# Optimization experiments

Measured on AMD Instinct MI355X. Metric: run time of the kernel, lower is better.

Reference implementation:

```python
import jax, jax.numpy as jnp
import numpy as np
from jax import lax

T_STEPS = 8

def _dwconv(x, kernel):
    # depthwise conv, NHWC input, HWIO kernel with I=1, groups=C
    C = x.shape[-1]
    return lax.conv_general_dilated(
        x, kernel, window_strides=(1, 1), padding='SAME',
        dimension_numbers=('NHWC', 'HWIO', 'NHWC'), feature_group_count=C)

def setup_inputs() -> dict:
    key = jax.random.key(0)
    k1, k2, k3 = jax.random.split(key, 3)
    B, H, W, C, k = 8, 128, 128, 256, 7
    x = jax.random.normal(k1, (B, H, W, C), dtype=jnp.float32)
    A_kernel = 0.02 * jax.random.normal(k2, (k, k, 1, C), dtype=jnp.float32)
    B_kernel = 0.02 * jax.random.normal(k3, (k, k, 1, C), dtype=jnp.float32)
    return {'x': x, 'A_kernel': A_kernel, 'B_kernel': B_kernel}

def reference(x, A_kernel, B_kernel):
    # SSM recurrence h_t = A * h_{t-1} + B * x  (depthwise spatial convs)
    A_stable = 0.9 * jnp.tanh(A_kernel)
    Bx = _dwconv(x, B_kernel)  # precomputed input drive, (B,H,W,C)

    def step(h, _):
        return _dwconv(h, A_stable) + Bx, None

    h0 = jnp.zeros_like(x)
    h_final, _ = lax.scan(step, h0, None, length=T_STEPS)
    return h_final
```

## Files before the change

kernel.cpp:

```cpp
#include <hip/hip_runtime.h>
#include <cmath>

#define HH    128
#define WW    128
#define CCH   256
#define BATCH 8
#define NPLANE (BATCH*CCH)
#define PLANE_ELEMS (HH*WW)

#define TB   3
#define STR  136
#define S4   34
#define HPAD 134
#define PLANE_LDS (HPAD*STR)

template<int SAVE_BX>
__device__ __forceinline__ void conv_pass(const float* src, float* dst,
                                          const float* cf, float* bx,
                                          int tx, int ty)
{
    const int x4 = tx * 2;
    const int y0 = ty * 8;
    __align__(16) float wd[7][16];
    const float4* s4 = (const float4*)src;
    float4* d4 = (float4*)dst;

#pragma unroll
    for (int r = 0; r < 7; r++) {
        const float4* row = s4 + (y0 + r) * S4 + x4;
        float4 a = row[0], b = row[1], c = row[2], d = row[3];
        *(float4*)&wd[r][0]  = a;  *(float4*)&wd[r][4]  = b;
        *(float4*)&wd[r][8]  = c;  *(float4*)&wd[r][12] = d;
    }

#pragma unroll
    for (int o = 0; o < 8; o++) {
        if (o > 0) {
            const int slot = (o + 6) % 7;
            const float4* row = s4 + (y0 + o + 6) * S4 + x4;
            float4 a = row[0], b = row[1], c = row[2], d = row[3];
            *(float4*)&wd[slot][0]  = a;  *(float4*)&wd[slot][4]  = b;
            *(float4*)&wd[slot][8]  = c;  *(float4*)&wd[slot][12] = d;
        }
        float acc[8];
#pragma unroll
        for (int i = 0; i < 8; i++) acc[i] = SAVE_BX ? 0.0f : bx[o * 8 + i];
#pragma unroll
        for (int ky = 0; ky < 7; ky++) {
            const int s = (o + ky) % 7;
#pragma unroll
            for (int kx = 0; kx < 7; kx++) {
                const float k = cf[ky * 7 + kx];
#pragma unroll
                for (int i = 0; i < 8; i++)
                    acc[i] = fmaf(wd[s][i + kx + 1], k, acc[i]);
            }
        }
        if (SAVE_BX) {
#pragma unroll
            for (int i = 0; i < 8; i++) bx[o * 8 + i] = acc[i];
        }
        float4 lo = make_float4(acc[0], acc[1], acc[2], acc[3]);
        float4 hi = make_float4(acc[4], acc[5], acc[6], acc[7]);
        float4* drow = d4 + (y0 + o + TB) * S4 + (tx * 2 + 1);
        drow[0] = lo;
        drow[1] = hi;
    }
}

__global__ __launch_bounds__(256, 1) void ssm_kernel(float* planes,
                                                     const float* __restrict__ Ak,
                                                     const float* __restrict__ Bk)
{
    __shared__ float buf[2 * PLANE_LDS];
    const int p  = blockIdx.x;
    const int c  = p & (CCH - 1);
    const int t  = threadIdx.x;
    const int tx = t & 15, ty = t >> 4;

    float4* z = (float4*)buf;
    const int n4 = 2 * PLANE_LDS / 4;
    for (int i = t; i < n4; i += 256) z[i] = make_float4(0.f, 0.f, 0.f, 0.f);

    float bco[49];
#pragma unroll
    for (int i = 0; i < 49; i++) bco[i] = Bk[i * CCH + c];

    __syncthreads();

    const float4* gx = (const float4*)planes + (size_t)p * (PLANE_ELEMS / 4);
#pragma unroll
    for (int i = 0; i < 16; i++) {
        int idx = i * 256 + t, y = idx >> 5, xc = idx & 31;
        ((float4*)buf)[(y + TB) * S4 + xc + 1] = gx[idx];
    }
    __syncthreads();

    float bx[64];
    conv_pass<1>(buf, buf + PLANE_LDS, bco, bx, tx, ty);

    float aco[49];
#pragma unroll
    for (int i = 0; i < 49; i++) {
        float v = 0.9f * tanhf(Ak[i * CCH + c]);
        aco[i] = __uint_as_float(__builtin_amdgcn_readfirstlane(__float_as_uint(v)));
    }
    __syncthreads();

    for (int s = 0; s < 7; s++) {
        const float* src = buf + (1 - (s & 1)) * PLANE_LDS;
        float* dst       = buf + (s & 1) * PLANE_LDS;
        conv_pass<0>(src, dst, aco, bx, tx, ty);
        __syncthreads();
    }

    float4* gout = (float4*)planes + (size_t)p * (PLANE_ELEMS / 4);
#pragma unroll
    for (int i = 0; i < 16; i++) {
        int idx = i * 256 + t, y = idx >> 5, xc = idx & 31;
        gout[idx] = ((float4*)buf)[(y + TB) * S4 + xc + 1];
    }
}

__global__ __launch_bounds__(256) void transpose_in(const float* __restrict__ x,
                                                    float* __restrict__ xt)
{
    __shared__ float tile[64][65];
    const int p = blockIdx.x;
    const int b = p >> 10, rem = p & 1023, thw = rem >> 2, tc = rem & 3;
    const int t = threadIdx.x;
    const int m = t & 15, g = t >> 4;

    const size_t inbase = ((size_t)(b * 16384 + thw * 64)) * 256 + tc * 64;
#pragma unroll
    for (int i = 0; i < 4; i++) {
        int r = i * 16 + g;
        float4 v = *(const float4*)(x + inbase + (size_t)r * 256 + m * 4);
        tile[r][m * 4 + 0] = v.x; tile[r][m * 4 + 1] = v.y;
        tile[r][m * 4 + 2] = v.z; tile[r][m * 4 + 3] = v.w;
    }
    __syncthreads();
    const size_t outbase = ((size_t)(b * 256 + tc * 64)) * 16384 + thw * 64;
#pragma unroll
    for (int i = 0; i < 4; i++) {
        int cr = i * 16 + g;
        float4 v = make_float4(tile[m * 4 + 0][cr], tile[m * 4 + 1][cr],
                               tile[m * 4 + 2][cr], tile[m * 4 + 3][cr]);
        *(float4*)(xt + outbase + (size_t)cr * 16384 + m * 4) = v;
    }
}

__global__ __launch_bounds__(256) void transpose_out(const float* __restrict__ ht,
                                                     float* __restrict__ out)
{
    __shared__ float tile[64][65];
    const int p = blockIdx.x;
    const int b = p >> 10, rem = p & 1023, thw = rem >> 2, tc = rem & 3;
    const int t = threadIdx.x;
    const int m = t & 15, g = t >> 4;

    const size_t inbase = ((size_t)(b * 256 + tc * 64)) * 16384 + thw * 64;
#pragma unroll
    for (int i = 0; i < 4; i++) {
        int cr = i * 16 + g;
        float4 v = *(const float4*)(ht + inbase + (size_t)cr * 16384 + m * 4);
        tile[cr][m * 4 + 0] = v.x; tile[cr][m * 4 + 1] = v.y;
        tile[cr][m * 4 + 2] = v.z; tile[cr][m * 4 + 3] = v.w;
    }
    __syncthreads();
    const size_t outbase = ((size_t)(b * 16384 + thw * 64)) * 256 + tc * 64;
#pragma unroll
    for (int i = 0; i < 4; i++) {
        int r = i * 16 + g;
        float4 v = make_float4(tile[m * 4 + 0][r], tile[m * 4 + 1][r],
                               tile[m * 4 + 2][r], tile[m * 4 + 3][r]);
        *(float4*)(out + outbase + (size_t)r * 256 + m * 4) = v;
    }
}

extern "C" void kernel_launch(void* const* d_in, const int* in_sizes, int n_in,
                              void* d_out, int out_size, void* d_ws, size_t ws_size,
                              hipStream_t stream)
{
    (void)in_sizes; (void)n_in; (void)out_size; (void)ws_size;
    const float* x  = (const float*)d_in[0];
    const float* Ak = (const float*)d_in[1];
    const float* Bk = (const float*)d_in[2];
    float* out    = (float*)d_out;
    float* planes = (float*)d_ws;

    transpose_in <<<8192, 256, 0, stream>>>(x, planes);
    ssm_kernel   <<<NPLANE, 256, 0, stream>>>(planes, Ak, Bk);
    transpose_out<<<8192, 256, 0, stream>>>(planes, out);
}
```

Measured before the change: 689.7 us.

## Single-buffer LDS with register staging to fit two blocks per CU

Switches the per-plane recurrence from two LDS buffers to one: each thread computes a 16x4 output tile into registers, syncs, then writes it back into the shared plane. The halved LDS footprint and launch bounds of 2 are meant to allow two blocks per CU so one block's LDS traffic can overlap the other's math. The final step writes straight from registers to global memory. The narrower 4-wide tile reloads more halo per output, and holding 64 bx plus 64 hn values per thread raises register pressure, which could cause spills.

```diff
diff --git a/kernel.cpp b/kernel.cpp
--- a/kernel.cpp
+++ b/kernel.cpp
@@ -14,77 +14,85 @@
 #define HPAD 134
 #define PLANE_LDS (HPAD*STR)
 
-template<int SAVE_BX>
-__device__ __forceinline__ void conv_pass(const float* src, float* dst,
-                                          const float* cf, float* bx,
-                                          int tx, int ty)
-{
-    const int x4 = tx * 2;
-    const int y0 = ty * 8;
-    __align__(16) float wd[7][16];
-    const float4* s4 = (const float4*)src;
-    float4* d4 = (float4*)dst;
+template<int INIT0>
+__device__ __forceinline__ void conv16(const float* sbuf, const float* cf,
+                                       const float* accin, float* out,
+                                       int tx, int ty)
+{
+    const int xq = tx;
+    const int y0 = ty * 16;
+    __align__(16) float wd[7][12];
+    const float4* s4 = (const float4*)sbuf;
 
 #pragma unroll
     for (int r = 0; r < 7; r++) {
-        const float4* row = s4 + (y0 + r) * S4 + x4;
-        float4 a = row[0], b = row[1], c = row[2], d = row[3];
-        *(float4*)&wd[r][0]  = a;  *(float4*)&wd[r][4]  = b;
-        *(float4*)&wd[r][8]  = c;  *(float4*)&wd[r][12] = d;
-    }
-
-#pragma unroll
-    for (int o = 0; o < 8; o++) {
+        const float4* row = s4 + (y0 + r) * S4 + xq;
+        float4 a = row[0], b = row[1], c = row[2];
+        *(float4*)&wd[r][0] = a; *(float4*)&wd[r][4] = b; *(float4*)&wd[r][8] = c;
+    }
+
+#pragma unroll
+    for (int o = 0; o < 16; o++) {
         if (o > 0) {
             const int slot = (o + 6) % 7;
-            const float4* row = s4 + (y0 + o + 6) * S4 + x4;
-            float4 a = row[0], b = row[1], c = row[2], d = row[3];
-            *(float4*)&wd[slot][0]  = a;  *(float4*)&wd[slot][4]  = b;
-            *(float4*)&wd[slot][8]  = c;  *(float4*)&wd[slot][12] = d;
+            const float4* row = s4 + (y0 + o + 6) * S4 + xq;
+            float4 a = row[0], b = row[1], c = row[2];
+            *(float4*)&wd[slot][0] = a; *(float4*)&wd[slot][4] = b;
+            *(float4*)&wd[slot][8] = c;
         }
-        float acc[8];
-#pragma unroll
-        for (int i = 0; i < 8; i++) acc[i] = SAVE_BX ? 0.0f : bx[o * 8 + i];
+        float a0, a1, a2, a3;
+        if (INIT0) { a0 = a1 = a2 = a3 = 0.0f; }
+        else { a0 = accin[o*4+0]; a1 = accin[o*4+1]; a2 = accin[o*4+2]; a3 = accin[o*4+3]; }
 #pragma unroll
         for (int ky = 0; ky < 7; ky++) {
             const int s = (o + ky) % 7;
 #pragma unroll
             for (int kx = 0; kx < 7; kx++) {
                 const float k = cf[ky * 7 + kx];
-#pragma unroll
-                for (int i = 0; i < 8; i++)
-                    acc[i] = fmaf(wd[s][i + kx + 1], k, acc[i]);
+                a0 = fmaf(wd[s][0 + kx + 1], k, a0);
+                a1 = fmaf(wd[s][1 + kx + 1], k, a1);
+                a2 = fmaf(wd[s][2 + kx + 1], k, a2);
+                a3 = fmaf(wd[s][3 + kx + 1], k, a3);
             }
         }
-        if (SAVE_BX) {
-#pragma unroll
-            for (int i = 0; i < 8; i++) bx[o * 8 + i] = acc[i];
-        }
-        float4 lo = make_float4(acc[0], acc[1], acc[2], acc[3]);
-        float4 hi = make_float4(acc[4], acc[5], acc[6], acc[7]);
-        float4* drow = d4 + (y0 + o + TB) * S4 + (tx * 2 + 1);
-        drow[0] = lo;
-        drow[1] = hi;
-    }
-}
-
-__global__ __launch_bounds__(256, 1) void ssm_kernel(float* planes,
+        out[o*4+0] = a0; out[o*4+1] = a1; out[o*4+2] = a2; out[o*4+3] = a3;
+    }
+}
+
+__device__ __forceinline__ void tile_to_lds(float* sbuf, const float* v,
+                                            int tx, int ty)
+{
+    float4* d4 = (float4*)sbuf;
+    const int y0 = ty * 16;
+#pragma unroll
+    for (int o = 0; o < 16; o++) {
+        d4[(y0 + o + TB) * S4 + tx + 1] =
+            make_float4(v[o*4+0], v[o*4+1], v[o*4+2], v[o*4+3]);
+    }
+}
+
+__global__ __launch_bounds__(256, 2) void ssm_kernel(float* planes,
                                                      const float* __restrict__ Ak,
                                                      const float* __restrict__ Bk)
 {
-    __shared__ float buf[2 * PLANE_LDS];
+    __shared__ float buf[PLANE_LDS];
     const int p  = blockIdx.x;
     const int c  = p & (CCH - 1);
     const int t  = threadIdx.x;
-    const int tx = t & 15, ty = t >> 4;
-
-    float4* z = (float4*)buf;
-    const int n4 = 2 * PLANE_LDS / 4;
-    for (int i = t; i < n4; i += 256) z[i] = make_float4(0.f, 0.f, 0.f, 0.f);
+    const int tx = t & 31, ty = t >> 5;
+
+    {
+        float4* z = (float4*)buf;
+        for (int i = t; i < PLANE_LDS / 4; i += 256)
+            z[i] = make_float4(0.f, 0.f, 0.f, 0.f);
+    }
 
     float bco[49];
 #pragma unroll
-    for (int i = 0; i < 49; i++) bco[i] = Bk[i * CCH + c];
+    for (int i = 0; i < 49; i++) {
+        float v = Bk[i * CCH + c];
+        bco[i] = __uint_as_float(__builtin_amdgcn_readfirstlane(__float_as_uint(v)));
+    }
 
     __syncthreads();
 
@@ -97,7 +105,7 @@
     __syncthreads();
 
     float bx[64];
-    conv_pass<1>(buf, buf + PLANE_LDS, bco, bx, tx, ty);
+    conv16<1>(buf, bco, nullptr, bx, tx, ty);
 
     float aco[49];
 #pragma unroll
@@ -105,20 +113,28 @@
         float v = 0.9f * tanhf(Ak[i * CCH + c]);
         aco[i] = __uint_as_float(__builtin_amdgcn_readfirstlane(__float_as_uint(v)));
     }
-    __syncthreads();
-
-    for (int s = 0; s < 7; s++) {
-        const float* src = buf + (1 - (s & 1)) * PLANE_LDS;
-        float* dst       = buf + (s & 1) * PLANE_LDS;
-        conv_pass<0>(src, dst, aco, bx, tx, ty);
+
+    __syncthreads();
+    tile_to_lds(buf, bx, tx, ty);
+    __syncthreads();
+
+    float hn[64];
+    for (int s = 0; s < 6; s++) {
+        conv16<0>(buf, aco, bx, hn, tx, ty);
         __syncthreads();
-    }
-
-    float4* gout = (float4*)planes + (size_t)p * (PLANE_ELEMS / 4);
-#pragma unroll
-    for (int i = 0; i < 16; i++) {
-        int idx = i * 256 + t, y = idx >> 5, xc = idx & 31;
-        gout[idx] = ((float4*)buf)[(y + TB) * S4 + xc + 1];
+        tile_to_lds(buf, hn, tx, ty);
+        __syncthreads();
+    }
+
+    conv16<0>(buf, aco, bx, hn, tx, ty);
+    {
+        float4* gout = (float4*)planes + (size_t)p * (PLANE_ELEMS / 4);
+        const int y0 = ty * 16;
+#pragma unroll
+        for (int o = 0; o < 16; o++) {
+            gout[(y0 + o) * 32 + tx] =
+                make_float4(hn[o*4+0], hn[o*4+1], hn[o*4+2], hn[o*4+3]);
+        }
     }
 }
 
```

After: 1.059 ms. +53.5%, slower.

## Use 512 threads per plane with 4-wide outputs and fuse final conv into store

Applied to the files above, without the earlier changes.

Doubles the threads per block to 512, so each thread computes 4 output columns instead of 8. This shrinks the sliding register window and the per-thread bx storage to lift occupancy and parallelism. The last recurrence step now writes straight to global memory instead of going through LDS and a separate copy-out loop. The cost is more redundant LDS window loads per output, since each 4-wide tile reloads 12 floats per row, and a higher thread count contending for the same LDS.

```diff
diff --git a/kernel.cpp b/kernel.cpp
--- a/kernel.cpp
+++ b/kernel.cpp
@@ -14,61 +14,54 @@
 #define HPAD 134
 #define PLANE_LDS (HPAD*STR)
 
-template<int SAVE_BX>
-__device__ __forceinline__ void conv_pass(const float* src, float* dst,
-                                          const float* cf, float* bx,
-                                          int tx, int ty)
+template<int MODE>
+__device__ __forceinline__ void conv8(const float* src, float* dstl, float4* gout,
+                                      const float* cf, float* bx, int tx, int ty)
 {
-    const int x4 = tx * 2;
     const int y0 = ty * 8;
-    __align__(16) float wd[7][16];
+    __align__(16) float wd[7][12];
     const float4* s4 = (const float4*)src;
-    float4* d4 = (float4*)dst;
+    float4* d4 = (float4*)dstl;
 
 #pragma unroll
     for (int r = 0; r < 7; r++) {
-        const float4* row = s4 + (y0 + r) * S4 + x4;
-        float4 a = row[0], b = row[1], c = row[2], d = row[3];
-        *(float4*)&wd[r][0]  = a;  *(float4*)&wd[r][4]  = b;
-        *(float4*)&wd[r][8]  = c;  *(float4*)&wd[r][12] = d;
+        const float4* row = s4 + (y0 + r) * S4 + tx;
+        float4 a = row[0], b = row[1], c = row[2];
+        *(float4*)&wd[r][0] = a; *(float4*)&wd[r][4] = b; *(float4*)&wd[r][8] = c;
     }
 
 #pragma unroll
     for (int o = 0; o < 8; o++) {
         if (o > 0) {
             const int slot = (o + 6) % 7;
-            const float4* row = s4 + (y0 + o + 6) * S4 + x4;
-            float4 a = row[0], b = row[1], c = row[2], d = row[3];
-            *(float4*)&wd[slot][0]  = a;  *(float4*)&wd[slot][4]  = b;
-            *(float4*)&wd[slot][8]  = c;  *(float4*)&wd[slot][12] = d;
+            const float4* row = s4 + (y0 + o + 6) * S4 + tx;
+            float4 a = row[0], b = row[1], c = row[2];
+            *(float4*)&wd[slot][0] = a; *(float4*)&wd[slot][4] = b;
+            *(float4*)&wd[slot][8] = c;
         }
-        float acc[8];
-#pragma unroll
-        for (int i = 0; i < 8; i++) acc[i] = SAVE_BX ? 0.0f : bx[o * 8 + i];
+        float a0, a1, a2, a3;
+        if (MODE == 0) { a0 = a1 = a2 = a3 = 0.0f; }
+        else { a0 = bx[o*4+0]; a1 = bx[o*4+1]; a2 = bx[o*4+2]; a3 = bx[o*4+3]; }
 #pragma unroll
         for (int ky = 0; ky < 7; ky++) {
             const int s = (o + ky) % 7;
 #pragma unroll
             for (int kx = 0; kx < 7; kx++) {
                 const float k = cf[ky * 7 + kx];
-#pragma unroll
-                for (int i = 0; i < 8; i++)
-                    acc[i] = fmaf(wd[s][i + kx + 1], k, acc[i]);
+                a0 = fmaf(wd[s][kx + 1], k, a0);
+                a1 = fmaf(wd[s][kx + 2], k, a1);
+                a2 = fmaf(wd[s][kx + 3], k, a2);
+                a3 = fmaf(wd[s][kx + 4], k, a3);
             }
         }
-        if (SAVE_BX) {
-#pragma unroll
-            for (int i = 0; i < 8; i++) bx[o * 8 + i] = acc[i];
-        }
-        float4 lo = make_float4(acc[0], acc[1], acc[2], acc[3]);
-        float4 hi = make_float4(acc[4], acc[5], acc[6], acc[7]);
-        float4* drow = d4 + (y0 + o + TB) * S4 + (tx * 2 + 1);
-        drow[0] = lo;
-        drow[1] = hi;
+        if (MODE == 0) { bx[o*4+0]=a0; bx[o*4+1]=a1; bx[o*4+2]=a2; bx[o*4+3]=a3; }
+        float4 v = make_float4(a0, a1, a2, a3);
+        if (MODE == 2) gout[(y0 + o) * 32 + tx] = v;
+        else           d4[(y0 + o + TB) * S4 + tx + 1] = v;
     }
 }
 
-__global__ __launch_bounds__(256, 1) void ssm_kernel(float* planes,
+__global__ __launch_bounds__(512, 2) void ssm_kernel(float* planes,
                                                      const float* __restrict__ Ak,
                                                      const float* __restrict__ Bk)
 {
@@ -76,30 +69,19 @@
     const int p  = blockIdx.x;
     const int c  = p & (CCH - 1);
     const int t  = threadIdx.x;
-    const int tx = t & 15, ty = t >> 4;
+    const int tx = t & 31, ty = t >> 5;
+    float* b0 = buf;
+    float* b1 = buf + PLANE_LDS;
 
-    float4* z = (float4*)buf;
-    const int n4 = 2 * PLANE_LDS / 4;
-    for (int i = t; i < n4; i += 256) z[i] = make_float4(0.f, 0.f, 0.f, 0.f);
+    {
+        float4* z = (float4*)buf;
+        for (int i = t; i < 2 * PLANE_LDS / 4; i += 512)
+            z[i] = make_float4(0.f, 0.f, 0.f, 0.f);
+    }
 
-    float bco[49];
+    float bco[49], aco[49];
 #pragma unroll
     for (int i = 0; i < 49; i++) bco[i] = Bk[i * CCH + c];
-
-    __syncthreads();
-
-    const float4* gx = (const float4*)planes + (size_t)p * (PLANE_ELEMS / 4);
-#pragma unroll
-    for (int i = 0; i < 16; i++) {
-        int idx = i * 256 + t, y = idx >> 5, xc = idx & 31;
-        ((float4*)buf)[(y + TB) * S4 + xc + 1] = gx[idx];
-    }
-    __syncthreads();
-
-    float bx[64];
-    conv_pass<1>(buf, buf + PLANE_LDS, bco, bx, tx, ty);
-
-    float aco[49];
 #pragma unroll
     for (int i = 0; i < 49; i++) {
         float v = 0.9f * tanhf(Ak[i * CCH + c]);
@@ -107,19 +89,27 @@
     }
     __syncthreads();
 
-    for (int s = 0; s < 7; s++) {
-        const float* src = buf + (1 - (s & 1)) * PLANE_LDS;
-        float* dst       = buf + (s & 1) * PLANE_LDS;
-        conv_pass<0>(src, dst, aco, bx, tx, ty);
+    const float4* gx = (const float4*)planes + (size_t)p * (PLANE_ELEMS / 4);
+#pragma unroll
+    for (int i = 0; i < 8; i++) {
+        int idx = i * 512 + t, y = idx >> 5, xc = idx & 31;
+        ((float4*)b0)[(y + TB) * S4 + xc + 1] = gx[idx];
+    }
+    __syncthreads();
+
+    float bx[32];
+    conv8<0>(b0, b1, nullptr, bco, bx, tx, ty);
+    __syncthreads();
+
+    for (int st = 0; st < 3; st++) {
+        conv8<1>(b1, b0, nullptr, aco, bx, tx, ty);
+        __syncthreads();
+        conv8<1>(b0, b1, nullptr, aco, bx, tx, ty);
         __syncthreads();
     }
 
     float4* gout = (float4*)planes + (size_t)p * (PLANE_ELEMS / 4);
-#pragma unroll
-    for (int i = 0; i < 16; i++) {
-        int idx = i * 256 + t, y = idx >> 5, xc = idx & 31;
-        gout[idx] = ((float4*)buf)[(y + TB) * S4 + xc + 1];
-    }
+    conv8<2>(b1, nullptr, gout, aco, bx, tx, ty);
 }
 
 __global__ __launch_bounds__(256) void transpose_in(const float* __restrict__ x,
@@ -190,6 +180,6 @@
     float* planes = (float*)d_ws;
 
     transpose_in <<<8192, 256, 0, stream>>>(x, planes);
-    ssm_kernel   <<<NPLANE, 256, 0, stream>>>(planes, Ak, Bk);
+    ssm_kernel   <<<NPLANE, 512, 0, stream>>>(planes, Ak, Bk);
     transpose_out<<<8192, 256, 0, stream>>>(planes, out);
 }
```

Result: no change. 683.4 us (-0.9%).
